# Optimization experiments

Hardware: AMD Instinct MI355X
Metric: run time of the kernel (lower is better)

The kernel has to match this reference:

```python
import jax, jax.numpy as jnp
import numpy as np

H = 128        # hidden_dim
HEADS = 4      # conv1 heads
NTYPE = 50     # node_type_num
MZN = 32       # model_zoo_num
MAXN = 64      # max_node_num
B = 16         # outer batch
G = B * MZN    # num graphs = 512
N = G * MAXN   # total nodes = 32768
E = N * 8      # edges = 262144


def layer_norm(x, g, b):
    mu = x.mean(-1, keepdims=True)
    var = ((x - mu) ** 2).mean(-1, keepdims=True)
    return (x - mu) / jnp.sqrt(var + 1e-6) * g + b


def gat_conv(x, src, dst, W, a_src, a_dst, bias):
    # PyG GATConv: lin (no bias) -> per-edge LeakyReLU(0.2) scores with
    # self-loops -> segment softmax over dst -> scatter-sum, concat heads + bias.
    n = x.shape[0]
    heads, c = a_src.shape
    xp = (x @ W).reshape(n, heads, c)              # [N,heads,c]
    al_s = (xp * a_src).sum(-1)                    # [N,heads]
    al_d = (xp * a_dst).sum(-1)                    # [N,heads]
    loop = jnp.arange(n)
    s = jnp.concatenate([src, loop])               # add self-loops
    d = jnp.concatenate([dst, loop])
    e = jax.nn.leaky_relu(al_s[s] + al_d[d], 0.2)  # [E+N,heads]
    m = jax.ops.segment_max(e, d, num_segments=n)
    ex = jnp.exp(e - m[d])
    denom = jax.ops.segment_sum(ex, d, num_segments=n)
    alpha = ex / denom[d]                          # segment softmax
    msg = xp[s] * alpha[:, :, None]                # [E+N,heads,c]
    out = jax.ops.segment_sum(msg, d, num_segments=n)
    return out.reshape(n, heads * c) + bias


def setup_inputs() -> dict:
    key = jax.random.key(0)
    ks = jax.random.split(key, 32)
    def rn(k, shape, s=0.05):
        return jax.random.normal(k, shape, jnp.float32) * s
    inp = {
        "t": jax.random.normal(ks[0], (G, 768), jnp.float32),
        "v": jax.random.normal(ks[1], (G, 768), jnp.float32),
        "m_idx": jax.random.randint(ks[2], (N,), 0, NTYPE + 1),
        "edge_index": jax.random.randint(ks[3], (2, E), 0, N),
        "Wt": rn(ks[4], (768, H)), "bt": jnp.zeros((H,), jnp.float32),
        "Wv": rn(ks[5], (768, H)), "bv": jnp.zeros((H,), jnp.float32),
        "emb": rn(ks[6], (NTYPE + 1, H), 1.0),
        "Wnode": rn(ks[7], (H, H)), "bnode": jnp.zeros((H,), jnp.float32),
        "Wstart": rn(ks[8], (2 * H, H)), "bstart": jnp.zeros((H,), jnp.float32),
        "ln_g": jnp.ones((H,), jnp.float32), "ln_b": jnp.zeros((H,), jnp.float32),
        "W1": rn(ks[9], (H, HEADS * H)),
        "a_src1": rn(ks[10], (HEADS, H)), "a_dst1": rn(ks[11], (HEADS, H)),
        "b1": jnp.zeros((HEADS * H,), jnp.float32),
        "W2": rn(ks[12], (HEADS * H, H)),
        "a_src2": rn(ks[13], (1, H)), "a_dst2": rn(ks[14], (1, H)),
        "b2": jnp.zeros((H,), jnp.float32),
        "Wo1": rn(ks[15], (H, H)), "bo1": jnp.zeros((H,), jnp.float32),
        "Wo2": rn(ks[16], (H, 1)), "bo2": jnp.zeros((1,), jnp.float32),
    }
    return inp


def reference(t, v, Wt, bt, Wv, bv, emb, Wnode, bnode, Wstart, bstart, ln_g, ln_b,
              W1, a_src1, a_dst1, b1, W2, a_src2, a_dst2, b2, Wo1, bo1, Wo2, bo2,
              m_idx, edge_index):
    te = t @ Wt + bt                               # [G,H]
    ve = v @ Wv + bv                               # [G,H]
    ne = emb[m_idx].reshape(G, MAXN, H)            # node type embeddings
    ne = ne @ Wnode + bnode
    start = jnp.concatenate([ve, te], axis=-1) @ Wstart + bstart
    ne = ne.at[:, 0].set(start).reshape(N, H)
    x = layer_norm(ne, ln_g, ln_b)
    src, dst = edge_index[0], edge_index[1]
    x = jax.nn.elu(gat_conv(x, src, dst, W1, a_src1, a_dst1, b1))  # [N,4H]
    x = jax.nn.elu(gat_conv(x, src, dst, W2, a_src2, a_dst2, b2))  # [N,H]
    mask = (m_idx >= 1).astype(x.dtype).reshape(G, MAXN, 1)
    pooled = (x.reshape(G, MAXN, H) * mask).sum(1) / mask.sum(1)   # masked mean
    h1 = jax.nn.leaky_relu(pooled.reshape(B, MZN, H) @ Wo1 + bo1, 0.01)
    logits = (h1 @ Wo2 + bo2).reshape(B, MZN)
    return logits
```

## Files before the change

### kernel.cpp

```cpp
#include <hip/hip_runtime.h>
#include <hip/hip_bf16.h>

typedef __hip_bfloat16 bf16;
typedef __attribute__((ext_vector_type(8))) short s8v;
typedef __attribute__((ext_vector_type(4))) float f4v;

#define NN 32768
#define EE 262144
#define GG 512
#define LDW 520

__device__ __forceinline__ float2 unpk(unsigned u) {
  float2 r;
  r.x = __uint_as_float(u << 16);
  r.y = __uint_as_float(u & 0xffff0000u);
  return r;
}
__device__ __forceinline__ unsigned pk(float x, float y) {
  union { bf16 h[2]; unsigned u; } p;
  p.h[0] = __float2bfloat16(x);
  p.h[1] = __float2bfloat16(y);
  return p.u;
}
__device__ __forceinline__ short f2bf_bits(float x) {
  bf16 h = __float2bfloat16(x);
  return *reinterpret_cast<short*>(&h);
}
__device__ __forceinline__ float wred_sum(float v) {
#pragma unroll
  for (int o = 32; o; o >>= 1) v += __shfl_xor(v, o, 64);
  return v;
}

__device__ __forceinline__ void packB_one(const float* W, int N, int K, int id, s8v* Bp) {
  int lane = id & 63;
  int tmp = id >> 6;
  int ksteps = K >> 5;
  int ks = tmp % ksteps;
  int nt = tmp / ksteps;
  int n = nt * 16 + (lane & 15);
  int kbase = ks * 32 + (lane >> 4) * 8;
  s8v r;
#pragma unroll
  for (int j = 0; j < 8; j++) r[j] = f2bf_bits(W[(size_t)(kbase + j) * N + n]);
  Bp[id] = r;
}

__global__ __launch_bounds__(256) void prep_kernel(
    const int* __restrict__ dst, int* __restrict__ indeg,
    const float* __restrict__ W1, s8v* __restrict__ Bp1,
    const float* __restrict__ W2, s8v* __restrict__ Bp2,
    const float* __restrict__ a_src1, const float* __restrict__ a_dst1,
    float* __restrict__ ws1, float* __restrict__ wd1,
    const float* __restrict__ emb, const float* __restrict__ Wnode,
    const float* __restrict__ bnode, bf16* __restrict__ emb2_b,
    const float* __restrict__ Wv, const float* __restrict__ Wt,
    const float* __restrict__ Ws,
    const float* __restrict__ bv, const float* __restrict__ bt,
    const float* __restrict__ bstart,
    float* __restrict__ Wvs, float* __restrict__ Wts,
    float* __restrict__ bs2) {
  int b = blockIdx.x, tid = threadIdx.x;
  if (b < 1024) {
    int e = b * 256 + tid;
    atomicAdd(&indeg[dst[e]], 1);
  } else if (b < 1056) {
    packB_one(W1, 512, 128, (b - 1024) * 256 + tid, Bp1);
  } else if (b < 1088) {
    packB_one(W2, 128, 512, (b - 1056) * 256 + tid, Bp2);
  } else if (b < 1090) {
    int id = (b - 1088) * 256 + tid;
    int h = id >> 7, k = id & 127;
    float s = 0.f, d = 0.f;
    for (int c = 0; c < 128; c++) {
      float w0 = W1[(size_t)k * 512 + h * 128 + c];
      s = fmaf(w0, a_src1[h * 128 + c], s);
      d = fmaf(w0, a_dst1[h * 128 + c], d);
    }
    ws1[id] = s;
    wd1[id] = d;
  } else if (b < 1192) {
    __shared__ float red[256];
    int bb = b - 1090;
    int lo = tid & 63, slice = tid >> 6;
    long oid = (long)bb * 64 + lo;
    bool live = (oid < 51L * 128);
    int m = 0, n = 0;
    if (live) { m = (int)(oid >> 7); n = (int)(oid & 127); }
    float acc = 0.f;
    if (live) {
      const float* Ar = emb + (size_t)m * 128;
      for (int k = slice * 32; k < slice * 32 + 32; k++)
        acc = fmaf(Ar[k], Wnode[(size_t)k * 128 + n], acc);
    }
    red[tid] = acc;
    __syncthreads();
    if (slice == 0 && live) {
      float v = red[lo] + red[64 + lo] + red[128 + lo] + red[192 + lo];
      emb2_b[(size_t)m * 128 + n] = __float2bfloat16(v + bnode[n]);
    }
  } else if (b < 1576) {
    int id = (b - 1192) * 256 + tid;
    bool isT = id >= 49152;
    int o = isT ? id - 49152 : id;
    int k = o >> 6, cp = o & 63, c0 = cp * 2;
    const float* Wrow = (isT ? Wt : Wv) + (size_t)k * 128;
    const float* Wsc = Ws + (isT ? (size_t)128 * 128 : 0);
    float s0 = 0.f, s1 = 0.f;
    for (int j = 0; j < 128; j++) {
      float w = Wrow[j];
      float2 q = *(const float2*)(Wsc + (size_t)j * 128 + c0);
      s0 = fmaf(w, q.x, s0);
      s1 = fmaf(w, q.y, s1);
    }
    float* dp = (isT ? Wts : Wvs) + (size_t)k * 128 + c0;
    dp[0] = s0;
    dp[1] = s1;
  } else {
    if (tid < 128) {
      float s = bstart[tid];
      for (int k = 0; k < 128; k++) {
        s = fmaf(bv[k], Ws[(size_t)k * 128 + tid], s);
        s = fmaf(bt[k], Ws[(size_t)(128 + k) * 128 + tid], s);
      }
      bs2[tid] = s;
    }
  }
}

__global__ __launch_bounds__(1024) void scan_start_kernel(
    const int* __restrict__ indeg, int* __restrict__ off, int* __restrict__ cursor,
    const float* __restrict__ tf, const float* __restrict__ vf,
    const float* __restrict__ Wvs, const float* __restrict__ Wts,
    const float* __restrict__ bs2, bf16* __restrict__ start_b) {
  int t = threadIdx.x;
  if (blockIdx.x == 0) {
    __shared__ int sh[1024];
    int loc[32];
    int s = 0;
    int base = t * 32;
#pragma unroll
    for (int j = 0; j < 32; j++) { loc[j] = indeg[base + j]; s += loc[j]; }
    sh[t] = s;
    __syncthreads();
    for (int d = 1; d < 1024; d <<= 1) {
      int v = (t >= d) ? sh[t - d] : 0;
      __syncthreads();
      sh[t] += v;
      __syncthreads();
    }
    int run = (t == 0) ? 0 : sh[t - 1];
#pragma unroll
    for (int j = 0; j < 32; j++) { off[base + j] = run; cursor[base + j] = run; run += loc[j]; }
    if (t == 1023) off[NN] = run;
    return;
  }
  __shared__ float red[1024];
  int g = blockIdx.x - 1;
  int c = t & 127, slice = t >> 7;
  const float* vrow = vf + (size_t)g * 768;
  const float* trow = tf + (size_t)g * 768;
  float acc = 0.f;
  int k0 = slice * 96;
#pragma unroll 4
  for (int k = k0; k < k0 + 96; k++)
    acc = fmaf(vrow[k], Wvs[(size_t)k * 128 + c], fmaf(trow[k], Wts[(size_t)k * 128 + c], acc));
  red[t] = acc;
  __syncthreads();
  if (t < 512) red[t] += red[t + 512];
  __syncthreads();
  if (t < 256) red[t] += red[t + 256];
  __syncthreads();
  if (t < 128) {
    float s = red[t] + red[t + 128] + bs2[t];
    start_b[(size_t)g * 128 + t] = __float2bfloat16(s);
  }
}

__global__ __launch_bounds__(256) void fill_ln_kernel(
    const int* __restrict__ src, const int* __restrict__ dst,
    int* __restrict__ cursor, int* __restrict__ esrc, int* __restrict__ edst,
    const unsigned* __restrict__ start_b, const unsigned* __restrict__ emb2_b,
    const int* __restrict__ m_idx, const float* __restrict__ lng,
    const float* __restrict__ lnb, const float* __restrict__ ws1,
    const float* __restrict__ wd1, unsigned* __restrict__ x0b,
    float* __restrict__ als, float* __restrict__ ald) {
  int b = blockIdx.x;
  if (b < 1024) {
    int e = b * 256 + threadIdx.x;
    int d = dst[e];
    int p = atomicAdd(&cursor[d], 1);
    esrc[p] = src[e];
    edst[p] = d;
    return;
  }
  int bb = b - 1024;
  int i = bb * 4 + (threadIdx.x >> 6);
  int lane = threadIdx.x & 63;
  int g = i >> 6, n = i & 63;
  const unsigned* row = (n == 0) ? (start_b + (size_t)g * 64) : (emb2_b + (size_t)m_idx[i] * 64);
  float2 v = unpk(row[lane]);
  float mu = wred_sum(v.x + v.y) * (1.f / 128.f);
  float dx = v.x - mu, dy = v.y - mu;
  float var = wred_sum(dx * dx + dy * dy) * (1.f / 128.f);
  float rstd = rsqrtf(var + 1e-6f);
  float2 gg = ((const float2*)lng)[lane];
  float2 bbv = ((const float2*)lnb)[lane];
  float xx = dx * rstd * gg.x + bbv.x;
  float xy = dy * rstd * gg.y + bbv.y;
  x0b[(size_t)i * 64 + lane] = pk(xx, xy);
#pragma unroll
  for (int h = 0; h < 4; h++) {
    float2 s2 = ((const float2*)(ws1 + h * 128))[lane];
    float2 d2 = ((const float2*)(wd1 + h * 128))[lane];
    float ps = wred_sum(xx * s2.x + xy * s2.y);
    float pd = wred_sum(xx * d2.x + xy * d2.y);
    if (lane == 0) { als[i * 4 + h] = ps; ald[i * 4 + h] = pd; }
  }
}

__global__ __launch_bounds__(256) void escore1_kernel(
    const float4* __restrict__ als4, const float4* __restrict__ ald4,
    const int* __restrict__ esrc, const int* __restrict__ edst,
    float4* __restrict__ aw4) {
  int p = blockIdx.x * 256 + threadIdx.x;
  float4 a = als4[esrc[p]];
  float4 d = ald4[edst[p]];
  float v0 = a.x + d.x, v1 = a.y + d.y, v2 = a.z + d.z, v3 = a.w + d.w;
  v0 = v0 > 0.f ? v0 : 0.2f * v0; v1 = v1 > 0.f ? v1 : 0.2f * v1;
  v2 = v2 > 0.f ? v2 : 0.2f * v2; v3 = v3 > 0.f ? v3 : 0.2f * v3;
  aw4[p] = make_float4(__expf(v0), __expf(v1), __expf(v2), __expf(v3));
}

__global__ __launch_bounds__(256) void escore2_kernel(
    const float* __restrict__ als, const float* __restrict__ ald,
    const int* __restrict__ esrc, const int* __restrict__ edst,
    float* __restrict__ aw) {
  int p = blockIdx.x * 256 + threadIdx.x;
  float sc = als[esrc[p]] + ald[edst[p]];
  sc = sc > 0.f ? sc : 0.2f * sc;
  aw[p] = __expf(sc);
}

__global__ __launch_bounds__(256) void conv12f_kernel(
    const uint4* __restrict__ x0,
    const float4* __restrict__ aw4,
    const float4* __restrict__ als4, const float4* __restrict__ ald4,
    const int* __restrict__ off, const int* __restrict__ esrc,
    const s8v* __restrict__ Bp1, const float* __restrict__ b1,
    const s8v* __restrict__ Bp2,
    const float* __restrict__ a_src2, const float* __restrict__ a_dst2,
    short* __restrict__ xp2, float* __restrict__ als2, float* __restrict__ ald2) {
  __shared__ short lds[64 * LDW];
  int tid = threadIdx.x;
  int brow = blockIdx.x * 64;
  {
    int c8 = tid & 15, rsub = tid >> 4;
    for (int grp = 0; grp < 4; grp++) {
      int i = brow + grp * 16 + rsub;
      float4 sa = als4[i], sd = ald4[i];
      float u0 = sa.x + sd.x, u1 = sa.y + sd.y, u2 = sa.z + sd.z, u3 = sa.w + sd.w;
      u0 = u0 > 0.f ? u0 : 0.2f * u0; u1 = u1 > 0.f ? u1 : 0.2f * u1;
      u2 = u2 > 0.f ? u2 : 0.2f * u2; u3 = u3 > 0.f ? u3 : 0.2f * u3;
      float sw0 = __expf(u0), sw1 = __expf(u1), sw2 = __expf(u2), sw3 = __expf(u3);
      float dn0 = sw0, dn1 = sw1, dn2 = sw2, dn3 = sw3;
      uint4 xv = x0[(size_t)i * 16 + c8];
      float x[8];
      { float2 p0 = unpk(xv.x), p1 = unpk(xv.y), p2 = unpk(xv.z), p3 = unpk(xv.w);
        x[0]=p0.x; x[1]=p0.y; x[2]=p1.x; x[3]=p1.y; x[4]=p2.x; x[5]=p2.y; x[6]=p3.x; x[7]=p3.y; }
      float acc[4][8];
#pragma unroll
      for (int j = 0; j < 8; j++) {
        acc[0][j] = sw0 * x[j]; acc[1][j] = sw1 * x[j];
        acc[2][j] = sw2 * x[j]; acc[3][j] = sw3 * x[j];
      }
      int e0 = off[i], e1 = off[i + 1];
      int e = e0;
      for (; e + 1 < e1; e += 2) {
        int sA = esrc[e], sB = esrc[e + 1];
        float4 wA = aw4[e], wB = aw4[e + 1];
        uint4 mA = x0[(size_t)sA * 16 + c8];
        uint4 mB = x0[(size_t)sB * 16 + c8];
        float2 q0 = unpk(mA.x), q1 = unpk(mA.y), q2 = unpk(mA.z), q3 = unpk(mA.w);
        float qa[8] = {q0.x, q0.y, q1.x, q1.y, q2.x, q2.y, q3.x, q3.y};
#pragma unroll
        for (int j = 0; j < 8; j++) {
          acc[0][j] = fmaf(wA.x, qa[j], acc[0][j]);
          acc[1][j] = fmaf(wA.y, qa[j], acc[1][j]);
          acc[2][j] = fmaf(wA.z, qa[j], acc[2][j]);
          acc[3][j] = fmaf(wA.w, qa[j], acc[3][j]);
        }
        dn0 += wA.x; dn1 += wA.y; dn2 += wA.z; dn3 += wA.w;
        q0 = unpk(mB.x); q1 = unpk(mB.y); q2 = unpk(mB.z); q3 = unpk(mB.w);
        float qb[8] = {q0.x, q0.y, q1.x, q1.y, q2.x, q2.y, q3.x, q3.y};
#pragma unroll
        for (int j = 0; j < 8; j++) {
          acc[0][j] = fmaf(wB.x, qb[j], acc[0][j]);
          acc[1][j] = fmaf(wB.y, qb[j], acc[1][j]);
          acc[2][j] = fmaf(wB.z, qb[j], acc[2][j]);
          acc[3][j] = fmaf(wB.w, qb[j], acc[3][j]);
        }
        dn0 += wB.x; dn1 += wB.y; dn2 += wB.z; dn3 += wB.w;
      }
      if (e < e1) {
        int sA = esrc[e];
        float4 wA = aw4[e];
        uint4 mA = x0[(size_t)sA * 16 + c8];
        float2 q0 = unpk(mA.x), q1 = unpk(mA.y), q2 = unpk(mA.z), q3 = unpk(mA.w);
        float qa[8] = {q0.x, q0.y, q1.x, q1.y, q2.x, q2.y, q3.x, q3.y};
#pragma unroll
        for (int j = 0; j < 8; j++) {
          acc[0][j] = fmaf(wA.x, qa[j], acc[0][j]);
          acc[1][j] = fmaf(wA.y, qa[j], acc[1][j]);
          acc[2][j] = fmaf(wA.z, qa[j], acc[2][j]);
          acc[3][j] = fmaf(wA.w, qa[j], acc[3][j]);
        }
        dn0 += wA.x; dn1 += wA.y; dn2 += wA.z; dn3 += wA.w;
      }
      float ivh[4] = {1.f / dn0, 1.f / dn1, 1.f / dn2, 1.f / dn3};
      int row = grp * 16 + rsub;
#pragma unroll
      for (int h = 0; h < 4; h++) {
        uint4 o;
        o.x = pk(acc[h][0] * ivh[h], acc[h][1] * ivh[h]);
        o.y = pk(acc[h][2] * ivh[h], acc[h][3] * ivh[h]);
        o.z = pk(acc[h][4] * ivh[h], acc[h][5] * ivh[h]);
        o.w = pk(acc[h][6] * ivh[h], acc[h][7] * ivh[h]);
        *(uint4*)(lds + row * LDW + h * 128 + c8 * 8) = o;
      }
    }
  }
  __syncthreads();
  int wv = tid >> 6, lane = tid & 63, quad = lane >> 4, l16 = lane & 15;
  int arow = (wv * 16 + l16) * LDW;
  for (int h = 0; h < 4; h++) {
    f4v acc[8] = {};
#pragma unroll
    for (int ks = 0; ks < 4; ks++) {
      s8v a = *(const s8v*)(lds + arow + h * 128 + ks * 32 + quad * 8);
#pragma unroll
      for (int nt = 0; nt < 8; nt++) {
        s8v bf = Bp1[(size_t)((h * 8 + nt) * 4 + ks) * 64 + lane];
        acc[nt] = __builtin_amdgcn_mfma_f32_16x16x32_bf16(a, bf, acc[nt], 0, 0, 0);
      }
    }
#pragma unroll
    for (int nt = 0; nt < 8; nt++) {
      float bb = b1[h * 128 + nt * 16 + l16];
#pragma unroll
      for (int r = 0; r < 4; r++) {
        float vv = acc[nt][r] + bb;
        vv = vv > 0.f ? vv : (__expf(vv) - 1.f);
        lds[(wv * 16 + quad * 4 + r) * LDW + h * 128 + nt * 16 + l16] = f2bf_bits(vv);
      }
    }
  }
  __syncthreads();
  f4v acc2[8] = {};
  for (int ks = 0; ks < 16; ks++) {
    s8v a = *(const s8v*)(lds + arow + ks * 32 + quad * 8);
#pragma unroll
    for (int nt = 0; nt < 8; nt++) {
      s8v bf = Bp2[(size_t)(nt * 16 + ks) * 64 + lane];
      acc2[nt] = __builtin_amdgcn_mfma_f32_16x16x32_bf16(a, bf, acc2[nt], 0, 0, 0);
    }
  }
#pragma unroll
  for (int nt = 0; nt < 8; nt++)
#pragma unroll
    for (int r = 0; r < 4; r++)
      lds[(wv * 16 + quad * 4 + r) * LDW + nt * 16 + l16] = f2bf_bits(acc2[nt][r]);
  float2 as = ((const float2*)a_src2)[lane];
  float2 ad = ((const float2*)a_dst2)[lane];
  for (int r = 0; r < 16; r++) {
    int row = wv * 16 + r;
    float2 x = unpk(*(const unsigned*)(lds + row * LDW + lane * 2));
    float ps = wred_sum(x.x * as.x + x.y * as.y);
    float pd = wred_sum(x.x * ad.x + x.y * ad.y);
    if (lane == 0) { als2[brow + row] = ps; ald2[brow + row] = pd; }
  }
  __syncthreads();
#pragma unroll
  for (int rep = 0; rep < 4; rep++) {
    int idx = rep * 256 + tid;
    int row = idx >> 4, c16 = idx & 15;
    uint4 val = *(const uint4*)(lds + row * LDW + c16 * 8);
    *(uint4*)(xp2 + (size_t)(brow + row) * 128 + c16 * 8) = val;
  }
}

__global__ __launch_bounds__(256) void tail2_kernel(
    const uint4* __restrict__ xp,
    const float* __restrict__ aw,
    const float* __restrict__ als, const float* __restrict__ ald,
    const int* __restrict__ off, const int* __restrict__ esrc,
    const float* __restrict__ b2, const int* __restrict__ m_idx,
    const float* __restrict__ Wo1, const float* __restrict__ bo1,
    const float* __restrict__ Wo2, const float* __restrict__ bo2,
    float* __restrict__ out) {
  __shared__ float x2t[64 * 132];
  __shared__ float maskf[64];
  __shared__ float pl[128];
  __shared__ float red[256];
  int g = blockIdx.x, tid = threadIdx.x;
  if (tid < 64) maskf[tid] = (m_idx[g * 64 + tid] >= 1) ? 1.f : 0.f;
  int c8 = tid & 15, rsub = tid >> 4;
  for (int grp = 0; grp < 4; grp++) {
    int i = g * 64 + grp * 16 + rsub;
    float selfSc = als[i] + ald[i];
    selfSc = selfSc > 0.f ? selfSc : 0.2f * selfSc;
    float sw = __expf(selfSc);
    float dnm = sw;
    uint4 xv = xp[(size_t)i * 16 + c8];
    float2 p0 = unpk(xv.x), p1 = unpk(xv.y), p2 = unpk(xv.z), p3 = unpk(xv.w);
    float a0 = sw * p0.x, a1 = sw * p0.y, a2 = sw * p1.x, a3 = sw * p1.y;
    float a4 = sw * p2.x, a5 = sw * p2.y, a6 = sw * p3.x, a7 = sw * p3.y;
    int s0 = off[i], s1 = off[i + 1];
    int e = s0;
    for (; e + 1 < s1; e += 2) {
      int sA = esrc[e], sB = esrc[e + 1];
      float wA = aw[e], wB = aw[e + 1];
      uint4 mA = xp[(size_t)sA * 16 + c8];
      uint4 mB = xp[(size_t)sB * 16 + c8];
      float2 q0 = unpk(mA.x), q1 = unpk(mA.y), q2 = unpk(mA.z), q3 = unpk(mA.w);
      a0 = fmaf(wA, q0.x, a0); a1 = fmaf(wA, q0.y, a1);
      a2 = fmaf(wA, q1.x, a2); a3 = fmaf(wA, q1.y, a3);
      a4 = fmaf(wA, q2.x, a4); a5 = fmaf(wA, q2.y, a5);
      a6 = fmaf(wA, q3.x, a6); a7 = fmaf(wA, q3.y, a7);
      dnm += wA;
      q0 = unpk(mB.x); q1 = unpk(mB.y); q2 = unpk(mB.z); q3 = unpk(mB.w);
      a0 = fmaf(wB, q0.x, a0); a1 = fmaf(wB, q0.y, a1);
      a2 = fmaf(wB, q1.x, a2); a3 = fmaf(wB, q1.y, a3);
      a4 = fmaf(wB, q2.x, a4); a5 = fmaf(wB, q2.y, a5);
      a6 = fmaf(wB, q3.x, a6); a7 = fmaf(wB, q3.y, a7);
      dnm += wB;
    }
    if (e < s1) {
      int sA = esrc[e];
      float wA = aw[e];
      uint4 mA = xp[(size_t)sA * 16 + c8];
      float2 q0 = unpk(mA.x), q1 = unpk(mA.y), q2 = unpk(mA.z), q3 = unpk(mA.w);
      a0 = fmaf(wA, q0.x, a0); a1 = fmaf(wA, q0.y, a1);
      a2 = fmaf(wA, q1.x, a2); a3 = fmaf(wA, q1.y, a3);
      a4 = fmaf(wA, q2.x, a4); a5 = fmaf(wA, q2.y, a5);
      a6 = fmaf(wA, q3.x, a6); a7 = fmaf(wA, q3.y, a7);
      dnm += wA;
    }
    float ivv = 1.f / dnm;
    float4 bb0 = ((const float4*)b2)[c8 * 2];
    float4 bb1 = ((const float4*)b2)[c8 * 2 + 1];
    a0 = a0 * ivv + bb0.x; a1 = a1 * ivv + bb0.y; a2 = a2 * ivv + bb0.z; a3 = a3 * ivv + bb0.w;
    a4 = a4 * ivv + bb1.x; a5 = a5 * ivv + bb1.y; a6 = a6 * ivv + bb1.z; a7 = a7 * ivv + bb1.w;
    a0 = a0 > 0.f ? a0 : (__expf(a0) - 1.f);
    a1 = a1 > 0.f ? a1 : (__expf(a1) - 1.f);
    a2 = a2 > 0.f ? a2 : (__expf(a2) - 1.f);
    a3 = a3 > 0.f ? a3 : (__expf(a3) - 1.f);
    a4 = a4 > 0.f ? a4 : (__expf(a4) - 1.f);
    a5 = a5 > 0.f ? a5 : (__expf(a5) - 1.f);
    a6 = a6 > 0.f ? a6 : (__expf(a6) - 1.f);
    a7 = a7 > 0.f ? a7 : (__expf(a7) - 1.f);
    float* dp = x2t + (grp * 16 + rsub) * 132 + c8 * 8;
    dp[0] = a0; dp[1] = a1; dp[2] = a2; dp[3] = a3;
    dp[4] = a4; dp[5] = a5; dp[6] = a6; dp[7] = a7;
  }
  __syncthreads();
  int c = tid & 127, half = tid >> 7;
  float pacc = 0.f;
  for (int n = half * 32; n < half * 32 + 32; n++) pacc += maskf[n] * x2t[n * 132 + c];
  red[tid] = pacc;
  __syncthreads();
  float cnt = 0.f;
  for (int n = 0; n < 64; n++) cnt += maskf[n];
  if (half == 0) pl[c] = (red[c] + red[c + 128]) / cnt;
  __syncthreads();
  float hacc = 0.f;
  for (int k = half * 64; k < half * 64 + 64; k++)
    hacc = fmaf(pl[k], Wo1[(size_t)k * 128 + c], hacc);
  red[tid] = hacc;
  __syncthreads();
  if (half == 0) {
    float hh = red[c] + red[c + 128] + bo1[c];
    hh = hh > 0.f ? hh : 0.01f * hh;
    red[c] = hh * Wo2[c];
  }
  __syncthreads();
  for (int d = 64; d; d >>= 1) {
    if (tid < d) red[tid] += red[tid + d];
    __syncthreads();
  }
  if (tid == 0) out[g] = red[0] + bo2[0];
}

extern "C" void kernel_launch(void* const* d_in, const int* in_sizes, int n_in, void* d_out,
                              int out_size, void* d_ws, size_t ws_size, hipStream_t stream) {
  (void)n_in; (void)out_size; (void)ws_size;
  bool dict_order = (in_sizes[2] == NN);
  int IM, IE, IF[25];
  if (dict_order) {
    IM = 2; IE = 3;
    const int f[25] = {0, 1, 4, 5, 6, 7, 8, 9, 10, 11, 12, 13, 14, 15, 16, 17, 18,
                       19, 20, 21, 22, 23, 24, 25, 26};
    for (int k = 0; k < 25; k++) IF[k] = f[k];
  } else {
    IM = 25; IE = 26;
    for (int k = 0; k < 25; k++) IF[k] = k;
  }
  const int* m_idx = (const int*)d_in[IM];
  const int* eidx = (const int*)d_in[IE];
  float* out = (float*)d_out;
  const int* e_src = eidx;
  const int* e_dst = eidx + EE;

  const float* t = (const float*)d_in[IF[0]];
  const float* v = (const float*)d_in[IF[1]];
  const float* Wt = (const float*)d_in[IF[2]];     const float* bt = (const float*)d_in[IF[3]];
  const float* Wv = (const float*)d_in[IF[4]];     const float* bv = (const float*)d_in[IF[5]];
  const float* emb = (const float*)d_in[IF[6]];
  const float* Wnode = (const float*)d_in[IF[7]];  const float* bnode = (const float*)d_in[IF[8]];
  const float* Wstart = (const float*)d_in[IF[9]]; const float* bstart = (const float*)d_in[IF[10]];
  const float* ln_g = (const float*)d_in[IF[11]];  const float* ln_b = (const float*)d_in[IF[12]];
  const float* W1 = (const float*)d_in[IF[13]];
  const float* a_src1 = (const float*)d_in[IF[14]]; const float* a_dst1 = (const float*)d_in[IF[15]];
  const float* b1 = (const float*)d_in[IF[16]];
  const float* W2 = (const float*)d_in[IF[17]];
  const float* a_src2 = (const float*)d_in[IF[18]]; const float* a_dst2 = (const float*)d_in[IF[19]];
  const float* b2 = (const float*)d_in[IF[20]];
  const float* Wo1 = (const float*)d_in[IF[21]];   const float* bo1 = (const float*)d_in[IF[22]];
  const float* Wo2 = (const float*)d_in[IF[23]];   const float* bo2 = (const float*)d_in[IF[24]];

  char* w = (char*)d_ws;
  bf16* x0b = (bf16*)w;
  bf16* xp2b = (bf16*)(w + ((size_t)8 << 20));
  size_t so = (size_t)16 << 20;
  bf16* emb2_b = (bf16*)(w + so); so += 51 * 128 * 2 + 256;
  bf16* start_b = (bf16*)(w + so); so += 512 * 128 * 2;
  float* als1 = (float*)(w + so); so += NN * 4 * 4;
  float* ald1 = (float*)(w + so); so += NN * 4 * 4;
  float* als2 = (float*)(w + so); so += NN * 4;
  float* ald2 = (float*)(w + so); so += NN * 4;
  float* aw1 = (float*)(w + so); so += EE * 4 * 4;
  float* aw2 = (float*)(w + so); so += EE * 4;
  float* ws1 = (float*)(w + so); so += 512 * 4;
  float* wd1 = (float*)(w + so); so += 512 * 4;
  float* Wvs = (float*)(w + so); so += 768 * 128 * 4;
  float* Wts = (float*)(w + so); so += 768 * 128 * 4;
  float* bs2 = (float*)(w + so); so += 512;
  int* indeg = (int*)(w + so); so += NN * 4;
  int* csroff = (int*)(w + so); so += (NN + 1) * 4 + 252;
  int* cursor = (int*)(w + so); so += NN * 4;
  int* esrc = (int*)(w + so); so += EE * 4;
  int* edst = (int*)(w + so); so += EE * 4;
  s8v* Bp1 = (s8v*)(w + so); so += 32 * 4 * 64 * 16;
  s8v* Bp2 = (s8v*)(w + so); so += 8 * 16 * 64 * 16;

  hipMemsetAsync(indeg, 0, NN * 4, stream);
  prep_kernel<<<1577, 256, 0, stream>>>(e_dst, indeg,
      W1, Bp1, W2, Bp2, a_src1, a_dst1, ws1, wd1,
      emb, Wnode, bnode, emb2_b,
      Wv, Wt, Wstart, bv, bt, bstart, Wvs, Wts, bs2);
  scan_start_kernel<<<513, 1024, 0, stream>>>(indeg, csroff, cursor,
      t, v, Wvs, Wts, bs2, start_b);
  fill_ln_kernel<<<9216, 256, 0, stream>>>(e_src, e_dst, cursor, esrc, edst,
      (const unsigned*)start_b, (const unsigned*)emb2_b, m_idx, ln_g, ln_b,
      ws1, wd1, (unsigned*)x0b, als1, ald1);
  escore1_kernel<<<EE / 256, 256, 0, stream>>>((const float4*)als1, (const float4*)ald1,
                                               esrc, edst, (float4*)aw1);
  conv12f_kernel<<<NN / 64, 256, 0, stream>>>((const uint4*)x0b,
      (const float4*)aw1, (const float4*)als1, (const float4*)ald1,
      csroff, esrc, Bp1, b1, Bp2, a_src2, a_dst2, (short*)xp2b, als2, ald2);
  escore2_kernel<<<EE / 256, 256, 0, stream>>>(als2, ald2, esrc, edst, aw2);
  tail2_kernel<<<GG, 256, 0, stream>>>((const uint4*)xp2b, aw2, als2, ald2,
      csroff, esrc, b2, m_idx, Wo1, bo1, Wo2, bo2, out);
}
```

Measured before the change: 293.5 us.

## Fuse layer-2 edge scoring into tail and halve conv tile rows

```diff
diff --git a/kernel.cpp b/kernel.cpp
--- a/kernel.cpp
+++ b/kernel.cpp
@@ -232,16 +232,6 @@
   aw4[p] = make_float4(__expf(v0), __expf(v1), __expf(v2), __expf(v3));
 }
 
-__global__ __launch_bounds__(256) void escore2_kernel(
-    const float* __restrict__ als, const float* __restrict__ ald,
-    const int* __restrict__ esrc, const int* __restrict__ edst,
-    float* __restrict__ aw) {
-  int p = blockIdx.x * 256 + threadIdx.x;
-  float sc = als[esrc[p]] + ald[edst[p]];
-  sc = sc > 0.f ? sc : 0.2f * sc;
-  aw[p] = __expf(sc);
-}
-
 __global__ __launch_bounds__(256) void conv12f_kernel(
     const uint4* __restrict__ x0,
     const float4* __restrict__ aw4,
@@ -251,12 +241,12 @@
     const s8v* __restrict__ Bp2,
     const float* __restrict__ a_src2, const float* __restrict__ a_dst2,
     short* __restrict__ xp2, float* __restrict__ als2, float* __restrict__ ald2) {
-  __shared__ short lds[64 * LDW];
+  __shared__ short lds[32 * LDW];
   int tid = threadIdx.x;
-  int brow = blockIdx.x * 64;
+  int brow = blockIdx.x * 32;
   {
     int c8 = tid & 15, rsub = tid >> 4;
-    for (int grp = 0; grp < 4; grp++) {
+    for (int grp = 0; grp < 2; grp++) {
       int i = brow + grp * 16 + rsub;
       float4 sa = als4[i], sd = ald4[i];
       float u0 = sa.x + sd.x, u1 = sa.y + sd.y, u2 = sa.z + sd.z, u3 = sa.w + sd.w;
@@ -332,8 +322,10 @@
   }
   __syncthreads();
   int wv = tid >> 6, lane = tid & 63, quad = lane >> 4, l16 = lane & 15;
-  int arow = (wv * 16 + l16) * LDW;
-  for (int h = 0; h < 4; h++) {
+  int rt = wv & 1, cH = wv >> 1;
+  int arow = (rt * 16 + l16) * LDW;
+  for (int hh = 0; hh < 2; hh++) {
+    int h = cH * 2 + hh;
     f4v acc[8] = {};
 #pragma unroll
     for (int ks = 0; ks < 4; ks++) {
@@ -351,37 +343,41 @@
       for (int r = 0; r < 4; r++) {
         float vv = acc[nt][r] + bb;
         vv = vv > 0.f ? vv : (__expf(vv) - 1.f);
-        lds[(wv * 16 + quad * 4 + r) * LDW + h * 128 + nt * 16 + l16] = f2bf_bits(vv);
-      }
-    }
-  }
-  __syncthreads();
-  f4v acc2[8] = {};
+        lds[(rt * 16 + quad * 4 + r) * LDW + h * 128 + nt * 16 + l16] = f2bf_bits(vv);
+      }
+    }
+  }
+  __syncthreads();
+  f4v acc2[4] = {};
   for (int ks = 0; ks < 16; ks++) {
     s8v a = *(const s8v*)(lds + arow + ks * 32 + quad * 8);
 #pragma unroll
-    for (int nt = 0; nt < 8; nt++) {
+    for (int j = 0; j < 4; j++) {
+      int nt = cH * 4 + j;
       s8v bf = Bp2[(size_t)(nt * 16 + ks) * 64 + lane];
-      acc2[nt] = __builtin_amdgcn_mfma_f32_16x16x32_bf16(a, bf, acc2[nt], 0, 0, 0);
-    }
-  }
-#pragma unroll
-  for (int nt = 0; nt < 8; nt++)
+      acc2[j] = __builtin_amdgcn_mfma_f32_16x16x32_bf16(a, bf, acc2[j], 0, 0, 0);
+    }
+  }
+  __syncthreads();
+#pragma unroll
+  for (int j = 0; j < 4; j++) {
+    int nt = cH * 4 + j;
 #pragma unroll
     for (int r = 0; r < 4; r++)
-      lds[(wv * 16 + quad * 4 + r) * LDW + nt * 16 + l16] = f2bf_bits(acc2[nt][r]);
+      lds[(rt * 16 + quad * 4 + r) * LDW + nt * 16 + l16] = f2bf_bits(acc2[j][r]);
+  }
+  __syncthreads();
   float2 as = ((const float2*)a_src2)[lane];
   float2 ad = ((const float2*)a_dst2)[lane];
-  for (int r = 0; r < 16; r++) {
-    int row = wv * 16 + r;
+  for (int r = 0; r < 8; r++) {
+    int row = wv * 8 + r;
     float2 x = unpk(*(const unsigned*)(lds + row * LDW + lane * 2));
     float ps = wred_sum(x.x * as.x + x.y * as.y);
     float pd = wred_sum(x.x * ad.x + x.y * ad.y);
     if (lane == 0) { als2[brow + row] = ps; ald2[brow + row] = pd; }
   }
-  __syncthreads();
-#pragma unroll
-  for (int rep = 0; rep < 4; rep++) {
+#pragma unroll
+  for (int rep = 0; rep < 2; rep++) {
     int idx = rep * 256 + tid;
     int row = idx >> 4, c16 = idx & 15;
     uint4 val = *(const uint4*)(lds + row * LDW + c16 * 8);
@@ -391,7 +387,6 @@
 
 __global__ __launch_bounds__(256) void tail2_kernel(
     const uint4* __restrict__ xp,
-    const float* __restrict__ aw,
     const float* __restrict__ als, const float* __restrict__ ald,
     const int* __restrict__ off, const int* __restrict__ esrc,
     const float* __restrict__ b2, const int* __restrict__ m_idx,
@@ -407,7 +402,8 @@
   int c8 = tid & 15, rsub = tid >> 4;
   for (int grp = 0; grp < 4; grp++) {
     int i = g * 64 + grp * 16 + rsub;
-    float selfSc = als[i] + ald[i];
+    float adi = ald[i];
+    float selfSc = als[i] + adi;
     selfSc = selfSc > 0.f ? selfSc : 0.2f * selfSc;
     float sw = __expf(selfSc);
     float dnm = sw;
@@ -419,7 +415,10 @@
     int e = s0;
     for (; e + 1 < s1; e += 2) {
       int sA = esrc[e], sB = esrc[e + 1];
-      float wA = aw[e], wB = aw[e + 1];
+      float scA = als[sA] + adi, scB = als[sB] + adi;
+      scA = scA > 0.f ? scA : 0.2f * scA;
+      scB = scB > 0.f ? scB : 0.2f * scB;
+      float wA = __expf(scA), wB = __expf(scB);
       uint4 mA = xp[(size_t)sA * 16 + c8];
       uint4 mB = xp[(size_t)sB * 16 + c8];
       float2 q0 = unpk(mA.x), q1 = unpk(mA.y), q2 = unpk(mA.z), q3 = unpk(mA.w);
@@ -437,7 +436,9 @@
     }
     if (e < s1) {
       int sA = esrc[e];
-      float wA = aw[e];
+      float scA = als[sA] + adi;
+      scA = scA > 0.f ? scA : 0.2f * scA;
+      float wA = __expf(scA);
       uint4 mA = xp[(size_t)sA * 16 + c8];
       float2 q0 = unpk(mA.x), q1 = unpk(mA.y), q2 = unpk(mA.z), q3 = unpk(mA.w);
       a0 = fmaf(wA, q0.x, a0); a1 = fmaf(wA, q0.y, a1);
@@ -539,7 +540,6 @@
   float* als2 = (float*)(w + so); so += NN * 4;
   float* ald2 = (float*)(w + so); so += NN * 4;
   float* aw1 = (float*)(w + so); so += EE * 4 * 4;
-  float* aw2 = (float*)(w + so); so += EE * 4;
   float* ws1 = (float*)(w + so); so += 512 * 4;
   float* wd1 = (float*)(w + so); so += 512 * 4;
   float* Wvs = (float*)(w + so); so += 768 * 128 * 4;
@@ -565,10 +565,9 @@
       ws1, wd1, (unsigned*)x0b, als1, ald1);
   escore1_kernel<<<EE / 256, 256, 0, stream>>>((const float4*)als1, (const float4*)ald1,
                                                esrc, edst, (float4*)aw1);
-  conv12f_kernel<<<NN / 64, 256, 0, stream>>>((const uint4*)x0b,
+  conv12f_kernel<<<NN / 32, 256, 0, stream>>>((const uint4*)x0b,
       (const float4*)aw1, (const float4*)als1, (const float4*)ald1,
       csroff, esrc, Bp1, b1, Bp2, a_src2, a_dst2, (short*)xp2b, als2, ald2);
-  escore2_kernel<<<EE / 256, 256, 0, stream>>>(als2, ald2, esrc, edst, aw2);
-  tail2_kernel<<<GG, 256, 0, stream>>>((const uint4*)xp2b, aw2, als2, ald2,
+  tail2_kernel<<<GG, 256, 0, stream>>>((const uint4*)xp2b, als2, ald2,
       csroff, esrc, b2, m_idx, Wo1, bo1, Wo2, bo2, out);
 }
```

After: 273.4 us. -6.9%, faster.
